# Kernel tuning notes

Hardware: AMD Instinct MI355X
Metric: run time of the kernel (lower is better)

## Reference

```python
import jax, jax.numpy as jnp
import numpy as np

H = 16
EPS = 1e-6
AUX_COEF = 0.01
TOPK = 2


def _rmsnorm(x, w):
    ms = jnp.mean(x * x, axis=-1, keepdims=True)
    return x * jax.lax.rsqrt(ms + EPS) * w


def _rope(t, cos, sin):
    # t: [B,H,T,hd]; cos/sin: [T, hd//2]
    half = t.shape[-1] // 2
    t1, t2 = t[..., :half], t[..., half:]
    return jnp.concatenate([t1 * cos - t2 * sin, t1 * sin + t2 * cos], axis=-1)


def setup_inputs() -> dict:
    key = jax.random.key(0)
    ks = jax.random.split(key, 16)
    B, T, D = 2, 1024, 1024
    E, I = 8, 4096
    s = lambda k, shp, fan: jax.random.normal(k, shp, dtype=jnp.float32) * (1.0 / np.sqrt(fan))
    return {
        "x": jax.random.normal(ks[0], (B, T, D), dtype=jnp.float32),
        "qkv_w": s(ks[1], (3 * D, D), D),
        "qkv_b": jnp.zeros((3 * D,), jnp.float32),
        "out_w": s(ks[2], (D, D), D),
        "out_b": jnp.zeros((D,), jnp.float32),
        "ln1_w": jnp.ones((D,), jnp.float32),
        "ln2_w": jnp.ones((D,), jnp.float32),
        "gate_w": s(ks[3], (E, D), D),
        "ew1": s(ks[4], (E, I, D), D),
        "eb1": jnp.zeros((E, I), jnp.float32),
        "ew2": s(ks[5], (E, D, I), I),
        "eb2": jnp.zeros((E, D), jnp.float32),
        "ew3": s(ks[6], (E, I, D), D),
        "eb3": jnp.zeros((E, I), jnp.float32),
    }


def _attention(x, qkv_w, qkv_b, out_w, out_b):
    B, T, D = x.shape
    hd = D // H
    half = hd // 2
    qkv = (x @ qkv_w.T + qkv_b).reshape(B, T, H, 3, hd)
    q = jnp.transpose(qkv[..., 0, :], (0, 2, 1, 3))  # [B,H,T,hd]
    k = jnp.transpose(qkv[..., 1, :], (0, 2, 1, 3))
    v = jnp.transpose(qkv[..., 2, :], (0, 2, 1, 3))
    theta = 1.0 / (10000.0 ** (jnp.arange(half, dtype=jnp.float32) / half))
    freq = jnp.arange(T, dtype=jnp.float32)[:, None] * theta[None, :]  # [T,half]
    cos, sin = jnp.cos(freq), jnp.sin(freq)
    q = _rope(q, cos, sin)
    k = _rope(k, cos, sin)
    # NOTE: original scales by embed_dim**-0.5 (not head_dim**-0.5)
    scale = D ** (-0.5)
    scores = jnp.einsum("bhqd,bhkd->bhqk", q, k) * scale
    mask = jnp.triu(jnp.full((T, T), -1e9, dtype=scores.dtype), k=1)
    w = jax.nn.softmax(scores + mask, axis=-1)
    attn = jnp.einsum("bhqk,bhkd->bhqd", w, v)
    attn = jnp.transpose(attn, (0, 2, 1, 3)).reshape(B, T, D)
    return attn @ out_w.T + out_b


def _moe(x, gate_w, ew1, eb1, ew2, eb2, ew3, eb3):
    B, T, D = x.shape
    E = gate_w.shape[0]
    xf = x.reshape(-1, D)  # [N,D]
    N = xf.shape[0]
    probs = jax.nn.softmax(xf @ gate_w.T, axis=-1)  # [N,E]
    topk_vals, topk_idx = jax.lax.top_k(probs, TOPK)
    oh = jax.nn.one_hot(topk_idx, E, dtype=xf.dtype)  # [N,K,E]
    gates = jnp.sum(oh * topk_vals[..., None], axis=1)  # [N,E] dense gate, zero off top-k
    # per-expert SwiGLU over all tokens, combined with sparse gates
    h = jax.nn.silu(jnp.einsum("nd,eid->nei", xf, ew1) + eb1) * (
        jnp.einsum("nd,eid->nei", xf, ew3) + eb3
    )  # [N,E,I]
    out_e = jnp.einsum("nei,edi->ned", h, ew2) + eb2  # [N,E,D]
    y = jnp.einsum("ned,ne->nd", out_e, gates)
    counts = jnp.sum(oh, axis=(0, 1))  # bincount of routed assignments
    f = counts / (N * TOPK)
    P = jnp.mean(probs, axis=0)
    aux = AUX_COEF * E * jnp.dot(f, P)
    return y.reshape(B, T, D), aux


def reference(x, qkv_w, qkv_b, out_w, out_b, ln1_w, ln2_w, gate_w, ew1, eb1, ew2, eb2, ew3, eb3):
    h1 = x + _attention(_rmsnorm(x, ln1_w), qkv_w, qkv_b, out_w, out_b)
    y, aux = _moe(_rmsnorm(h1, ln2_w), gate_w, ew1, eb1, ew2, eb2, ew3, eb3)
    return h1 + y, aux
```

## Files before the change

kernel.cpp:

```cpp
#include <hip/hip_runtime.h>
#include <cstdint>
#include <cstddef>
#include <math.h>

#define T_SEQ  1024
#define DMODEL 1024
#define NHEAD  16
#define HDIM   64
#define NEXP   8
#define IDIM   4096
#define NTOK   2048
#define NSLOT  4096

typedef short bf16x8 __attribute__((ext_vector_type(8)));
typedef short s16x4  __attribute__((ext_vector_type(4)));
typedef float floatx4 __attribute__((ext_vector_type(4)));
typedef unsigned int uintx4 __attribute__((ext_vector_type(4)));

__device__ __forceinline__ float bf2f(short s) {
  return __uint_as_float(((unsigned)(unsigned short)s) << 16);
}
__device__ __forceinline__ short f2bf(float f) {
  unsigned u = __float_as_uint(f);
  unsigned r = (u + 0x7FFFu + ((u >> 16) & 1u)) >> 16;
  return (short)r;
}
__device__ __forceinline__ unsigned cvt_pk_bf16(float lo, float hi) {
  unsigned r;
  asm("v_cvt_pk_bf16_f32 %0, %1, %2" : "=v"(r) : "v"(lo), "v"(hi));
  return r;
}
__device__ __forceinline__ uintx4 pack8_bf16(floatx4 a, floatx4 b) {
  uintx4 u;
  u[0] = cvt_pk_bf16(a[0], a[1]);
  u[1] = cvt_pk_bf16(a[2], a[3]);
  u[2] = cvt_pk_bf16(b[0], b[1]);
  u[3] = cvt_pk_bf16(b[2], b[3]);
  return u;
}
__device__ __forceinline__ void split8(const float* x, uintx4& hi, uintx4& lo) {
  #pragma unroll
  for (int i = 0; i < 4; i++) {
    unsigned h = cvt_pk_bf16(x[2*i], x[2*i+1]);
    hi[i] = h;
    float r0 = x[2*i]   - __uint_as_float(h << 16);
    float r1 = x[2*i+1] - __uint_as_float(h & 0xffff0000u);
    lo[i] = cvt_pk_bf16(r0, r1);
  }
}

__global__ __launch_bounds__(256) void rmsnorm_f32_kernel(
    const float* __restrict__ x, const float* __restrict__ w, float* __restrict__ out) {
  int row = blockIdx.x, tid = threadIdx.x;
  const floatx4* xr = (const floatx4*)(x + (size_t)row * DMODEL);
  floatx4 v = xr[tid];
  float ss = v[0]*v[0] + v[1]*v[1] + v[2]*v[2] + v[3]*v[3];
  #pragma unroll
  for (int off = 32; off > 0; off >>= 1) ss += __shfl_xor(ss, off);
  __shared__ float wsum[4];
  int wid = tid >> 6;
  if ((tid & 63) == 0) wsum[wid] = ss;
  __syncthreads();
  float tot = wsum[0] + wsum[1] + wsum[2] + wsum[3];
  float r = rsqrtf(tot * (1.0f / DMODEL) + 1e-6f);
  floatx4 wv = ((const floatx4*)w)[tid];
  floatx4 o;
  o[0] = v[0]*r*wv[0]; o[1] = v[1]*r*wv[1];
  o[2] = v[2]*r*wv[2]; o[3] = v[3]*r*wv[3];
  ((floatx4*)(out + (size_t)row * DMODEL))[tid] = o;
}

__global__ __launch_bounds__(256) void rmsnorm_bf16_kernel(
    const float* __restrict__ x, const float* __restrict__ w, short* __restrict__ out) {
  int row = blockIdx.x, tid = threadIdx.x;
  const floatx4* xr = (const floatx4*)(x + (size_t)row * DMODEL);
  floatx4 v = xr[tid];
  float ss = v[0]*v[0] + v[1]*v[1] + v[2]*v[2] + v[3]*v[3];
  #pragma unroll
  for (int off = 32; off > 0; off >>= 1) ss += __shfl_xor(ss, off);
  __shared__ float wsum[4];
  int wid = tid >> 6;
  if ((tid & 63) == 0) wsum[wid] = ss;
  __syncthreads();
  float tot = wsum[0] + wsum[1] + wsum[2] + wsum[3];
  float r = rsqrtf(tot * (1.0f / DMODEL) + 1e-6f);
  floatx4 wv = ((const floatx4*)w)[tid];
  s16x4 o;
  o[0] = f2bf(v[0]*r*wv[0]); o[1] = f2bf(v[1]*r*wv[1]);
  o[2] = f2bf(v[2]*r*wv[2]); o[3] = f2bf(v[3]*r*wv[3]);
  *(s16x4*)(out + (size_t)row * DMODEL + tid*4) = o;
}

template<int RESID>
__global__ __launch_bounds__(256) void gemm_3bf16(
    const float* __restrict__ A, const float* __restrict__ W,
    const float* __restrict__ bias, const float* __restrict__ resid,
    float* __restrict__ C, int N, int K) {
  __shared__ __attribute__((aligned(16))) short Ahi[64*40];
  __shared__ __attribute__((aligned(16))) short Alo[64*40];
  __shared__ __attribute__((aligned(16))) short Whi[64*40];
  __shared__ __attribute__((aligned(16))) short Wlo[64*40];
  int tid = threadIdx.x, lane = tid & 63, wid = tid >> 6;
  int wm = wid >> 1, wn = wid & 1;
  int m0 = blockIdx.y * 64, n0 = blockIdx.x * 64;
  floatx4 zero4 = {0.f,0.f,0.f,0.f};
  floatx4 acc[2][2];
  #pragma unroll
  for (int mi = 0; mi < 2; mi++)
    #pragma unroll
    for (int nj = 0; nj < 2; nj++) acc[mi][nj] = zero4;

  int ar = tid >> 2, ak = (tid & 3) * 8;
  const float* Ap = A + (size_t)(m0 + ar) * K + ak;
  const float* Wp = W + (size_t)(n0 + ar) * K + ak;
  int rsel = lane & 15, kseg = (lane >> 4) * 8;

  for (int kk = 0; kk < K; kk += 32) {
    float abuf[8], wbuf[8];
    *(floatx4*)(abuf)     = *(const floatx4*)(Ap + kk);
    *(floatx4*)(abuf + 4) = *(const floatx4*)(Ap + kk + 4);
    *(floatx4*)(wbuf)     = *(const floatx4*)(Wp + kk);
    *(floatx4*)(wbuf + 4) = *(const floatx4*)(Wp + kk + 4);
    uintx4 ahi, alo, whi, wlo;
    split8(abuf, ahi, alo);
    split8(wbuf, whi, wlo);
    __syncthreads();
    *(uintx4*)(&Ahi[ar*40 + ak]) = ahi;
    *(uintx4*)(&Alo[ar*40 + ak]) = alo;
    *(uintx4*)(&Whi[ar*40 + ak]) = whi;
    *(uintx4*)(&Wlo[ar*40 + ak]) = wlo;
    __syncthreads();
    bf16x8 afh[2], afl[2], wfh[2], wfl[2];
    #pragma unroll
    for (int mi = 0; mi < 2; mi++) {
      int row = (wm*32 + mi*16 + rsel)*40 + kseg;
      afh[mi] = *(const bf16x8*)(&Ahi[row]);
      afl[mi] = *(const bf16x8*)(&Alo[row]);
    }
    #pragma unroll
    for (int nj = 0; nj < 2; nj++) {
      int row = (wn*32 + nj*16 + rsel)*40 + kseg;
      wfh[nj] = *(const bf16x8*)(&Whi[row]);
      wfl[nj] = *(const bf16x8*)(&Wlo[row]);
    }
    #pragma unroll
    for (int mi = 0; mi < 2; mi++)
      #pragma unroll
      for (int nj = 0; nj < 2; nj++) {
        acc[mi][nj] = __builtin_amdgcn_mfma_f32_16x16x32_bf16(afl[mi], wfh[nj], acc[mi][nj], 0, 0, 0);
        acc[mi][nj] = __builtin_amdgcn_mfma_f32_16x16x32_bf16(afh[mi], wfl[nj], acc[mi][nj], 0, 0, 0);
        acc[mi][nj] = __builtin_amdgcn_mfma_f32_16x16x32_bf16(afh[mi], wfh[nj], acc[mi][nj], 0, 0, 0);
      }
  }
  int rj = (lane >> 4) * 4, cn = lane & 15;
  #pragma unroll
  for (int mi = 0; mi < 2; mi++) {
    #pragma unroll
    for (int nj = 0; nj < 2; nj++) {
      int n = n0 + wn*32 + nj*16 + cn;
      float bn = bias[n];
      #pragma unroll
      for (int j = 0; j < 4; j++) {
        int m = m0 + wm*32 + mi*16 + rj + j;
        float v = acc[mi][nj][j] + bn;
        if (RESID) v += resid[(size_t)m * N + n];
        C[(size_t)m * N + n] = v;
      }
    }
  }
}

__global__ void rope_table_kernel(float* __restrict__ cost, float* __restrict__ sint) {
  int t = blockIdx.x, d = threadIdx.x;
  double theta = pow(10000.0, -(double)d / 32.0);
  double f = (double)t * theta;
  cost[t*32 + d] = (float)cos(f);
  sint[t*32 + d] = (float)sin(f);
}

__global__ __launch_bounds__(256) void rope_kernel(
    const float* __restrict__ qkv, const float* __restrict__ cost, const float* __restrict__ sint,
    float* __restrict__ qr, float* __restrict__ kr) {
  int wid = threadIdx.x >> 6, lane = threadIdx.x & 63;
  int idx = blockIdx.x * 4 + wid;
  int h = idx & 15, n = idx >> 4;
  int t = n & (T_SEQ - 1), b = n >> 10;
  const float* base = qkv + (size_t)n * 3072 + h * 192;
  int d2 = lane & 31;
  float c = cost[t*32 + d2], s = sint[t*32 + d2];
  float q1 = base[d2],      q2 = base[d2 + 32];
  float k1 = base[64 + d2], k2 = base[96 + d2];
  float qo = (lane < 32) ? (q1*c - q2*s) : (q1*s + q2*c);
  float ko = (lane < 32) ? (k1*c - k2*s) : (k1*s + k2*c);
  size_t orow = ((size_t)(b*NHEAD + h) * T_SEQ + t) * HDIM;
  qr[orow + lane] = qo;
  kr[orow + lane] = ko;
}

__global__ __launch_bounds__(256) void vtrans_kernel(
    const float* __restrict__ qkvf, float* __restrict__ vrT) {
  __shared__ __attribute__((aligned(16))) float tile[64][68];
  int bh = blockIdx.x, t0 = blockIdx.y * 64;
  int b = bh >> 4, h = bh & 15;
  int tid = threadIdx.x;
  int r = tid >> 2, seg = (tid & 3) * 16;
  const float* src = qkvf + ((size_t)(b*T_SEQ + t0 + r))*3072 + h*192 + 128 + seg;
  floatx4 v0 = *(const floatx4*)(src);
  floatx4 v1 = *(const floatx4*)(src + 4);
  floatx4 v2 = *(const floatx4*)(src + 8);
  floatx4 v3 = *(const floatx4*)(src + 12);
  *(floatx4*)(&tile[r][seg])      = v0;
  *(floatx4*)(&tile[r][seg + 4])  = v1;
  *(floatx4*)(&tile[r][seg + 8])  = v2;
  *(floatx4*)(&tile[r][seg + 12]) = v3;
  __syncthreads();
  int dr = r, tseg = seg;
  floatx4 o0, o1, o2, o3;
  #pragma unroll
  for (int i = 0; i < 4; i++) {
    o0[i] = tile[tseg + i][dr];
    o1[i] = tile[tseg + 4 + i][dr];
    o2[i] = tile[tseg + 8 + i][dr];
    o3[i] = tile[tseg + 12 + i][dr];
  }
  float* dst = vrT + ((size_t)(bh*HDIM + dr))*T_SEQ + t0 + tseg;
  *(floatx4*)(dst)      = o0;
  *(floatx4*)(dst + 4)  = o1;
  *(floatx4*)(dst + 8)  = o2;
  *(floatx4*)(dst + 12) = o3;
}

__global__ __launch_bounds__(256) void attn_mfma_kernel(
    const float* __restrict__ qr_, const float* __restrict__ kr_,
    const float* __restrict__ vrT_, float* __restrict__ attno) {
  __shared__ __attribute__((aligned(16))) short Qhi[64*72];
  __shared__ __attribute__((aligned(16))) short Qlo[64*72];
  __shared__ __attribute__((aligned(16))) short Khi[64*72];
  __shared__ __attribute__((aligned(16))) short Klo[64*72];
  __shared__ __attribute__((aligned(16))) short Vhi[64*72];
  __shared__ __attribute__((aligned(16))) short Vlo[64*72];
  __shared__ __attribute__((aligned(16))) unsigned Pp[64*68];
  int tid = threadIdx.x, lane = tid & 63, w = tid >> 6;
  int bh = blockIdx.x;
  int qt = 15 - (int)blockIdx.y;
  int q0 = qt * 64;
  int b = bh >> 4, h = bh & 15;
  const float* Qb  = qr_  + ((size_t)bh * T_SEQ + q0) * HDIM;
  const float* Kb  = kr_  + (size_t)bh * T_SEQ * HDIM;
  const float* Vtb = vrT_ + (size_t)bh * HDIM * T_SEQ;

  int srow = tid >> 2, sseg = (tid & 3) * 16;
  {
    const float* src = Qb + srow*HDIM + sseg;
    float b0[8], b1[8];
    *(floatx4*)(b0)   = *(const floatx4*)(src);
    *(floatx4*)(b0+4) = *(const floatx4*)(src + 4);
    *(floatx4*)(b1)   = *(const floatx4*)(src + 8);
    *(floatx4*)(b1+4) = *(const floatx4*)(src + 12);
    uintx4 h0, l0, h1, l1;
    split8(b0, h0, l0); split8(b1, h1, l1);
    *(uintx4*)(&Qhi[srow*72 + sseg])     = h0;
    *(uintx4*)(&Qhi[srow*72 + sseg + 8]) = h1;
    *(uintx4*)(&Qlo[srow*72 + sseg])     = l0;
    *(uintx4*)(&Qlo[srow*72 + sseg + 8]) = l1;
  }

  int rsel = lane & 15, kseg = (lane >> 4) * 8, cl = lane & 15;
  int rbase = w*16 + (lane >> 4) * 4;
  const float scale = 0.03125f;
  float mrow[4] = {-1e30f,-1e30f,-1e30f,-1e30f};
  float lrow[4] = {0.f,0.f,0.f,0.f};
  floatx4 zero4 = {0.f,0.f,0.f,0.f};
  floatx4 Of[4];
  #pragma unroll
  for (int f = 0; f < 4; f++) Of[f] = zero4;

  int ntiles = qt + 1;
  for (int kt = 0; kt < ntiles; kt++) {
    int kbase = kt << 6;
    const float* kp = Kb  + (size_t)(kbase + srow)*HDIM + sseg;
    const float* vp = Vtb + (size_t)srow*T_SEQ + kbase + sseg;
    float kb0[8], kb1[8], vb0[8], vb1[8];
    *(floatx4*)(kb0)   = *(const floatx4*)(kp);
    *(floatx4*)(kb0+4) = *(const floatx4*)(kp + 4);
    *(floatx4*)(kb1)   = *(const floatx4*)(kp + 8);
    *(floatx4*)(kb1+4) = *(const floatx4*)(kp + 12);
    *(floatx4*)(vb0)   = *(const floatx4*)(vp);
    *(floatx4*)(vb0+4) = *(const floatx4*)(vp + 4);
    *(floatx4*)(vb1)   = *(const floatx4*)(vp + 8);
    *(floatx4*)(vb1+4) = *(const floatx4*)(vp + 12);
    __syncthreads();
    {
      uintx4 h0, l0, h1, l1;
      split8(kb0, h0, l0); split8(kb1, h1, l1);
      *(uintx4*)(&Khi[srow*72 + sseg])     = h0;
      *(uintx4*)(&Khi[srow*72 + sseg + 8]) = h1;
      *(uintx4*)(&Klo[srow*72 + sseg])     = l0;
      *(uintx4*)(&Klo[srow*72 + sseg + 8]) = l1;
      split8(vb0, h0, l0); split8(vb1, h1, l1);
      *(uintx4*)(&Vhi[srow*72 + sseg])     = h0;
      *(uintx4*)(&Vhi[srow*72 + sseg + 8]) = h1;
      *(uintx4*)(&Vlo[srow*72 + sseg])     = l0;
      *(uintx4*)(&Vlo[srow*72 + sseg + 8]) = l1;
    }
    __syncthreads();
    floatx4 sf[4];
    #pragma unroll
    for (int f = 0; f < 4; f++) sf[f] = zero4;
    #pragma unroll
    for (int c = 0; c < 2; c++) {
      int ko = c*32 + kseg;
      bf16x8 qh = *(const bf16x8*)(&Qhi[(w*16 + rsel)*72 + ko]);
      bf16x8 ql = *(const bf16x8*)(&Qlo[(w*16 + rsel)*72 + ko]);
      #pragma unroll
      for (int f = 0; f < 4; f++) {
        bf16x8 kh = *(const bf16x8*)(&Khi[(f*16 + rsel)*72 + ko]);
        bf16x8 kl = *(const bf16x8*)(&Klo[(f*16 + rsel)*72 + ko]);
        sf[f] = __builtin_amdgcn_mfma_f32_16x16x32_bf16(ql, kh, sf[f], 0, 0, 0);
        sf[f] = __builtin_amdgcn_mfma_f32_16x16x32_bf16(qh, kl, sf[f], 0, 0, 0);
        sf[f] = __builtin_amdgcn_mfma_f32_16x16x32_bf16(qh, kh, sf[f], 0, 0, 0);
      }
    }
    float pm[4] = {-1e30f,-1e30f,-1e30f,-1e30f};
    #pragma unroll
    for (int f = 0; f < 4; f++) {
      int col = kbase + f*16 + cl;
      #pragma unroll
      for (int j = 0; j < 4; j++) {
        float s = sf[f][j];
        s = (col <= q0 + rbase + j) ? s*scale : -1e30f;
        sf[f][j] = s;
        pm[j] = fmaxf(pm[j], s);
      }
    }
    #pragma unroll
    for (int off = 1; off < 16; off <<= 1)
      #pragma unroll
      for (int j = 0; j < 4; j++) pm[j] = fmaxf(pm[j], __shfl_xor(pm[j], off));
    float sc[4], rs[4] = {0.f,0.f,0.f,0.f};
    #pragma unroll
    for (int j = 0; j < 4; j++) {
      float mn = fmaxf(mrow[j], pm[j]);
      sc[j] = __expf(mrow[j] - mn);
      mrow[j] = mn;
    }
    #pragma unroll
    for (int f = 0; f < 4; f++) {
      #pragma unroll
      for (int j = 0; j < 4; j++) {
        float p = (sf[f][j] > -1e29f) ? __expf(sf[f][j] - mrow[j]) : 0.f;
        rs[j] += p;
        unsigned hp = cvt_pk_bf16(p, 0.f);
        float ph = __uint_as_float(hp << 16);
        unsigned lp = cvt_pk_bf16(p - ph, 0.f);
        Pp[(rbase + j)*68 + f*16 + cl] = (hp << 16) | (lp & 0xffffu);
      }
    }
    #pragma unroll
    for (int off = 1; off < 16; off <<= 1)
      #pragma unroll
      for (int j = 0; j < 4; j++) rs[j] += __shfl_xor(rs[j], off);
    #pragma unroll
    for (int j = 0; j < 4; j++) lrow[j] = lrow[j]*sc[j] + rs[j];
    #pragma unroll
    for (int f = 0; f < 4; f++)
      #pragma unroll
      for (int j = 0; j < 4; j++) Of[f][j] *= sc[j];
    __syncthreads();
    #pragma unroll
    for (int c = 0; c < 2; c++) {
      int prow = (w*16 + rsel)*68 + c*32 + kseg;
      uintx4 d0 = *(const uintx4*)(&Pp[prow]);
      uintx4 d1 = *(const uintx4*)(&Pp[prow + 4]);
      uintx4 phw, plw;
      phw[0] = (d0[0] >> 16) | (d0[1] & 0xffff0000u);
      phw[1] = (d0[2] >> 16) | (d0[3] & 0xffff0000u);
      phw[2] = (d1[0] >> 16) | (d1[1] & 0xffff0000u);
      phw[3] = (d1[2] >> 16) | (d1[3] & 0xffff0000u);
      plw[0] = (d0[0] & 0xffffu) | (d0[1] << 16);
      plw[1] = (d0[2] & 0xffffu) | (d0[3] << 16);
      plw[2] = (d1[0] & 0xffffu) | (d1[1] << 16);
      plw[3] = (d1[2] & 0xffffu) | (d1[3] << 16);
      bf16x8 Ph = *(bf16x8*)&phw;
      bf16x8 Pl = *(bf16x8*)&plw;
      int ko = c*32 + kseg;
      #pragma unroll
      for (int f = 0; f < 4; f++) {
        bf16x8 vh = *(const bf16x8*)(&Vhi[(f*16 + rsel)*72 + ko]);
        bf16x8 vl = *(const bf16x8*)(&Vlo[(f*16 + rsel)*72 + ko]);
        Of[f] = __builtin_amdgcn_mfma_f32_16x16x32_bf16(Pl, vh, Of[f], 0, 0, 0);
        Of[f] = __builtin_amdgcn_mfma_f32_16x16x32_bf16(Ph, vl, Of[f], 0, 0, 0);
        Of[f] = __builtin_amdgcn_mfma_f32_16x16x32_bf16(Ph, vh, Of[f], 0, 0, 0);
      }
    }
  }
  #pragma unroll
  for (int j = 0; j < 4; j++) {
    float inv = 1.0f / lrow[j];
    size_t rowoff = ((size_t)(b*T_SEQ + q0 + rbase + j))*DMODEL + h*HDIM;
    #pragma unroll
    for (int f = 0; f < 4; f++)
      attno[rowoff + f*16 + cl] = Of[f][j] * inv;
  }
}

__global__ __launch_bounds__(64) void gate_kernel(
    const float* __restrict__ h1, const float* __restrict__ lnw, const float* __restrict__ gw,
    float* __restrict__ probs, int* __restrict__ pair, float* __restrict__ gpair,
    int* __restrict__ counts) {
  int n = blockIdx.x, lane = threadIdx.x;
  const float* xp = h1 + (size_t)n * DMODEL + lane*16;
  float xv[16];
  double ss = 0.0;
  #pragma unroll
  for (int j = 0; j < 16; j++) { xv[j] = xp[j]; ss += (double)xv[j] * (double)xv[j]; }
  #pragma unroll
  for (int off = 32; off > 0; off >>= 1) ss += __shfl_xor(ss, off);
  double r = 1.0 / sqrt(ss * (1.0 / DMODEL) + 1e-6);
  const float* wp = lnw + lane*16;
  double xf[16];
  #pragma unroll
  for (int j = 0; j < 16; j++) xf[j] = (double)xv[j] * r * (double)wp[j];
  double logit[8];
  #pragma unroll
  for (int e = 0; e < 8; e++) {
    const float* g = gw + e*DMODEL + lane*16;
    double acc = 0.0;
    #pragma unroll
    for (int j = 0; j < 16; j++) acc += xf[j] * (double)g[j];
    logit[e] = acc;
  }
  #pragma unroll
  for (int e = 0; e < 8; e++)
    #pragma unroll
    for (int off = 32; off > 0; off >>= 1) logit[e] += __shfl_xor(logit[e], off);
  double mxl = logit[0];
  #pragma unroll
  for (int e = 1; e < 8; e++) mxl = fmax(mxl, logit[e]);
  double p[8], Z = 0.0;
  #pragma unroll
  for (int e = 0; e < 8; e++) { p[e] = exp(logit[e] - mxl); Z += p[e]; }
  double invZ = 1.0 / Z;
  #pragma unroll
  for (int e = 0; e < 8; e++) p[e] *= invZ;
  int e0 = 0; double b0 = p[0];
  #pragma unroll
  for (int e = 1; e < 8; e++) if (p[e] > b0) { b0 = p[e]; e0 = e; }
  int e1 = -1; double b1 = -1.0;
  #pragma unroll
  for (int e = 0; e < 8; e++) if (e != e0 && p[e] > b1) { b1 = p[e]; e1 = e; }
  if (lane == 0) {
    #pragma unroll
    for (int e = 0; e < 8; e++) probs[n*8 + e] = (float)p[e];
    pair[2*n] = e0; pair[2*n+1] = e1;
    gpair[2*n] = (float)b0; gpair[2*n+1] = (float)b1;
    atomicAdd(&counts[e0], 1);
    atomicAdd(&counts[e1], 1);
  }
}

__global__ void offsets_kernel(const int* __restrict__ counts, int* __restrict__ off,
                               int* __restrict__ cursor) {
  if (threadIdx.x == 0) {
    int a = 0;
    for (int e = 0; e < 8; e++) { off[e] = a; cursor[e] = a; a += counts[e]; }
    off[8] = a;
  }
}

__global__ __launch_bounds__(256) void scatter_kernel(
    const int* __restrict__ pair, const float* __restrict__ gpair, int* __restrict__ cursor,
    int* __restrict__ tok_of_slot, float* __restrict__ gate_of_slot, int* __restrict__ slot_of_tok) {
  int n = blockIdx.x * 256 + threadIdx.x;
  int e0 = pair[2*n], e1 = pair[2*n+1];
  int s0 = atomicAdd(&cursor[e0], 1);
  tok_of_slot[s0] = n; gate_of_slot[s0] = gpair[2*n];   slot_of_tok[2*n] = s0;
  int s1 = atomicAdd(&cursor[e1], 1);
  tok_of_slot[s1] = n; gate_of_slot[s1] = gpair[2*n+1]; slot_of_tok[2*n+1] = s1;
}

__global__ __launch_bounds__(256) void aux_kernel(
    const float* __restrict__ probs, const int* __restrict__ counts, float* __restrict__ outaux) {
  __shared__ double sm[256];
  int t = threadIdx.x;
  int e = t & 7, base = t >> 3;
  double acc = 0.0;
  for (int n = base; n < NTOK; n += 32) acc += (double)probs[n*8 + e];
  sm[t] = acc;
  __syncthreads();
  if (t < 8) {
    double s = 0.0;
    for (int g = 0; g < 32; g++) s += sm[g*8 + t];
    sm[t] = s;
  }
  __syncthreads();
  if (t == 0) {
    double aux = 0.0;
    for (int ee = 0; ee < 8; ee++)
      aux += ((double)counts[ee] * (1.0 / (NTOK*2))) * (sm[ee] * (1.0 / NTOK));
    outaux[0] = (float)(0.08 * aux);
  }
}

__global__ __launch_bounds__(256) void moe13_kernel(
    const short* __restrict__ xn2,
    const float* __restrict__ ew1, const float* __restrict__ eb1,
    const float* __restrict__ ew3, const float* __restrict__ eb3,
    const int* __restrict__ counts, const int* __restrict__ off,
    const int* __restrict__ tok_of_slot, short* __restrict__ hbuf) {
  int e = blockIdx.z;
  int Me = counts[e];
  int m0 = blockIdx.y * 128;
  if (m0 >= Me) return;
  int base = off[e];
  int i0 = blockIdx.x * 64;
  __shared__ __attribute__((aligned(16))) short As[2][128*40];
  __shared__ __attribute__((aligned(16))) short W1s[2][64*40];
  __shared__ __attribute__((aligned(16))) short W3s[2][64*40];
  int tid = threadIdx.x, lane = tid & 63, wid = tid >> 6;
  int wm = wid >> 1, wn = wid & 1;
  floatx4 zero4 = {0.f,0.f,0.f,0.f};
  floatx4 acc1[4][2], acc3[4][2];
  #pragma unroll
  for (int mi = 0; mi < 4; mi++)
    #pragma unroll
    for (int nj = 0; nj < 2; nj++) { acc1[mi][nj] = zero4; acc3[mi][nj] = zero4; }

  int ar = tid >> 1, ak = (tid & 1) * 8;
  int am = m0 + ar;
  bool aval = (am < Me);
  const short* Ag = xn2 + (size_t)(aval ? tok_of_slot[base + am] : 0) * DMODEL;
  int wr = tid >> 2, wk = (tid & 3) * 8;
  const float* W1g = ew1 + ((size_t)e*IDIM + i0 + wr)*DMODEL + wk;
  const float* W3g = ew3 + ((size_t)e*IDIM + i0 + wr)*DMODEL + wk;
  int rsel = lane & 15, kseg = (lane >> 4) * 8;

  {
    bf16x8 a0 = {0,0,0,0,0,0,0,0}, a1 = {0,0,0,0,0,0,0,0};
    if (aval) {
      a0 = *(const bf16x8*)(Ag + ak);
      a1 = *(const bf16x8*)(Ag + ak + 16);
    }
    floatx4 u0 = *(const floatx4*)(W1g);
    floatx4 u1 = *(const floatx4*)(W1g + 4);
    floatx4 v0 = *(const floatx4*)(W3g);
    floatx4 v1 = *(const floatx4*)(W3g + 4);
    *(bf16x8*)(&As[0][ar*40 + ak])      = a0;
    *(bf16x8*)(&As[0][ar*40 + ak + 16]) = a1;
    *(uintx4*)(&W1s[0][wr*40 + wk]) = pack8_bf16(u0, u1);
    *(uintx4*)(&W3s[0][wr*40 + wk]) = pack8_bf16(v0, v1);
  }
  __syncthreads();

  for (int kk = 0; kk < DMODEL; kk += 32) {
    int cur = (kk >> 5) & 1;
    int nxt = cur ^ 1;
    bool more = (kk + 32 < DMODEL);
    bf16x8 na0 = {0,0,0,0,0,0,0,0}, na1 = {0,0,0,0,0,0,0,0};
    floatx4 nu0, nu1, nv0, nv1;
    if (more) {
      if (aval) {
        na0 = *(const bf16x8*)(Ag + kk + 32 + ak);
        na1 = *(const bf16x8*)(Ag + kk + 32 + ak + 16);
      }
      nu0 = *(const floatx4*)(W1g + kk + 32);
      nu1 = *(const floatx4*)(W1g + kk + 36);
      nv0 = *(const floatx4*)(W3g + kk + 32);
      nv1 = *(const floatx4*)(W3g + kk + 36);
    }
    bf16x8 af[4], w1f[2], w3f[2];
    #pragma unroll
    for (int mi = 0; mi < 4; mi++)
      af[mi] = *(const bf16x8*)(&As[cur][(wm*64 + mi*16 + rsel)*40 + kseg]);
    #pragma unroll
    for (int nj = 0; nj < 2; nj++) {
      w1f[nj] = *(const bf16x8*)(&W1s[cur][(wn*32 + nj*16 + rsel)*40 + kseg]);
      w3f[nj] = *(const bf16x8*)(&W3s[cur][(wn*32 + nj*16 + rsel)*40 + kseg]);
    }
    #pragma unroll
    for (int mi = 0; mi < 4; mi++)
      #pragma unroll
      for (int nj = 0; nj < 2; nj++) {
        acc1[mi][nj] = __builtin_amdgcn_mfma_f32_16x16x32_bf16(af[mi], w1f[nj], acc1[mi][nj], 0, 0, 0);
        acc3[mi][nj] = __builtin_amdgcn_mfma_f32_16x16x32_bf16(af[mi], w3f[nj], acc3[mi][nj], 0, 0, 0);
      }
    if (more) {
      *(bf16x8*)(&As[nxt][ar*40 + ak])      = na0;
      *(bf16x8*)(&As[nxt][ar*40 + ak + 16]) = na1;
      *(uintx4*)(&W1s[nxt][wr*40 + wk]) = pack8_bf16(nu0, nu1);
      *(uintx4*)(&W3s[nxt][wr*40 + wk]) = pack8_bf16(nv0, nv1);
    }
    __syncthreads();
  }
  int rj = (lane >> 4) * 4, cn = lane & 15;
  #pragma unroll
  for (int mi = 0; mi < 4; mi++) {
    #pragma unroll
    for (int nj = 0; nj < 2; nj++) {
      int i = i0 + wn*32 + nj*16 + cn;
      float be1 = eb1[e*IDIM + i], be3 = eb3[e*IDIM + i];
      #pragma unroll
      for (int j = 0; j < 4; j++) {
        int m = m0 + wm*64 + mi*16 + rj + j;
        if (m < Me) {
          float a = acc1[mi][nj][j] + be1;
          float b = acc3[mi][nj][j] + be3;
          float hval = (a / (1.f + __expf(-a))) * b;
          hbuf[(size_t)(base + m)*IDIM + i] = f2bf(hval);
        }
      }
    }
  }
}

__global__ __launch_bounds__(256) void moe2_kernel(
    const short* __restrict__ hbuf, const float* __restrict__ ew2, const float* __restrict__ eb2,
    const int* __restrict__ counts, const int* __restrict__ off,
    const float* __restrict__ gate_of_slot,
    float* __restrict__ y0, float* __restrict__ y1) {
  int e = blockIdx.z;
  int Me = counts[e];
  int m0 = blockIdx.y * 128;
  if (m0 >= Me) return;
  int base = off[e];
  int n0 = (blockIdx.x & 7) * 128;
  int khalf = blockIdx.x >> 3;
  int kbeg = khalf * (IDIM/2);
  __shared__ __attribute__((aligned(16))) short As[2][128*40];
  __shared__ __attribute__((aligned(16))) short Ws[2][128*40];
  int tid = threadIdx.x, lane = tid & 63, wid = tid >> 6;
  int wm = wid >> 1, wn = wid & 1;
  floatx4 zero4 = {0.f,0.f,0.f,0.f};
  floatx4 acc[4][4];
  #pragma unroll
  for (int mi = 0; mi < 4; mi++)
    #pragma unroll
    for (int nj = 0; nj < 4; nj++) acc[mi][nj] = zero4;

  int ar = tid >> 1, ak = (tid & 1) * 8, kw = (tid & 1) * 16;
  bool aval = (m0 + ar) < Me;
  const short* Ag = hbuf + (size_t)(base + (aval ? (m0 + ar) : 0)) * IDIM + kbeg;
  const float* Wg = ew2 + ((size_t)e*DMODEL + n0 + ar)*IDIM + kbeg;
  int rsel = lane & 15, kseg = (lane >> 4) * 8;

  {
    bf16x8 a0 = {0,0,0,0,0,0,0,0}, a1 = {0,0,0,0,0,0,0,0};
    if (aval) {
      a0 = *(const bf16x8*)(Ag + ak);
      a1 = *(const bf16x8*)(Ag + ak + 16);
    }
    floatx4 w0 = *(const floatx4*)(Wg + kw);
    floatx4 w1 = *(const floatx4*)(Wg + kw + 4);
    floatx4 w2 = *(const floatx4*)(Wg + kw + 8);
    floatx4 w3 = *(const floatx4*)(Wg + kw + 12);
    *(bf16x8*)(&As[0][ar*40 + ak])      = a0;
    *(bf16x8*)(&As[0][ar*40 + ak + 16]) = a1;
    *(uintx4*)(&Ws[0][ar*40 + kw])     = pack8_bf16(w0, w1);
    *(uintx4*)(&Ws[0][ar*40 + kw + 8]) = pack8_bf16(w2, w3);
  }
  __syncthreads();

  for (int kk = 0; kk < IDIM/2; kk += 32) {
    int cur = (kk >> 5) & 1;
    int nxt = cur ^ 1;
    bool more = (kk + 32 < IDIM/2);
    bf16x8 na0 = {0,0,0,0,0,0,0,0}, na1 = {0,0,0,0,0,0,0,0};
    floatx4 nw0, nw1, nw2, nw3;
    if (more) {
      if (aval) {
        na0 = *(const bf16x8*)(Ag + kk + 32 + ak);
        na1 = *(const bf16x8*)(Ag + kk + 32 + ak + 16);
      }
      nw0 = *(const floatx4*)(Wg + kk + 32 + kw);
      nw1 = *(const floatx4*)(Wg + kk + 32 + kw + 4);
      nw2 = *(const floatx4*)(Wg + kk + 32 + kw + 8);
      nw3 = *(const floatx4*)(Wg + kk + 32 + kw + 12);
    }
    bf16x8 af[4], wf[4];
    #pragma unroll
    for (int mi = 0; mi < 4; mi++)
      af[mi] = *(const bf16x8*)(&As[cur][(wm*64 + mi*16 + rsel)*40 + kseg]);
    #pragma unroll
    for (int nj = 0; nj < 4; nj++)
      wf[nj] = *(const bf16x8*)(&Ws[cur][(wn*64 + nj*16 + rsel)*40 + kseg]);
    #pragma unroll
    for (int mi = 0; mi < 4; mi++)
      #pragma unroll
      for (int nj = 0; nj < 4; nj++)
        acc[mi][nj] = __builtin_amdgcn_mfma_f32_16x16x32_bf16(af[mi], wf[nj], acc[mi][nj], 0, 0, 0);
    if (more) {
      *(bf16x8*)(&As[nxt][ar*40 + ak])      = na0;
      *(bf16x8*)(&As[nxt][ar*40 + ak + 16]) = na1;
      *(uintx4*)(&Ws[nxt][ar*40 + kw])     = pack8_bf16(nw0, nw1);
      *(uintx4*)(&Ws[nxt][ar*40 + kw + 8]) = pack8_bf16(nw2, nw3);
    }
    __syncthreads();
  }
  int rj = (lane >> 4) * 4, cn = lane & 15;
  float* yout = khalf ? y1 : y0;
  #pragma unroll
  for (int mi = 0; mi < 4; mi++) {
    #pragma unroll
    for (int nj = 0; nj < 4; nj++) {
      int n = n0 + wn*64 + nj*16 + cn;
      float bn = khalf ? 0.f : eb2[e*DMODEL + n];
      #pragma unroll
      for (int j = 0; j < 4; j++) {
        int m = m0 + wm*64 + mi*16 + rj + j;
        if (m < Me) {
          float g = gate_of_slot[base + m];
          yout[(size_t)(base + m)*DMODEL + n] = (acc[mi][nj][j] + bn) * g;
        }
      }
    }
  }
}

__global__ __launch_bounds__(256) void combine_kernel(
    const float* __restrict__ h1, const float* __restrict__ y0, const float* __restrict__ y1,
    const int* __restrict__ slot_of_tok, float* __restrict__ out) {
  int n = blockIdx.x, t = threadIdx.x;
  int sA = slot_of_tok[2*n], sB = slot_of_tok[2*n+1];
  const floatx4* a   = (const floatx4*)(h1 + (size_t)n*DMODEL);
  const floatx4* y0a = (const floatx4*)(y0 + (size_t)sA*DMODEL);
  const floatx4* y1a = (const floatx4*)(y1 + (size_t)sA*DMODEL);
  const floatx4* y0b = (const floatx4*)(y0 + (size_t)sB*DMODEL);
  const floatx4* y1b = (const floatx4*)(y1 + (size_t)sB*DMODEL);
  floatx4 v = a[t] + (y0a[t] + y1a[t]) + (y0b[t] + y1b[t]);
  ((floatx4*)(out + (size_t)n*DMODEL))[t] = v;
}

extern "C" void kernel_launch(void* const* d_in, const int* in_sizes, int n_in,
                              void* d_out, int out_size, void* d_ws, size_t ws_size,
                              hipStream_t stream) {
  const float* x      = (const float*)d_in[0];
  const float* qkv_w  = (const float*)d_in[1];
  const float* qkv_b  = (const float*)d_in[2];
  const float* out_w  = (const float*)d_in[3];
  const float* out_b  = (const float*)d_in[4];
  const float* ln1_w  = (const float*)d_in[5];
  const float* ln2_w  = (const float*)d_in[6];
  const float* gate_w = (const float*)d_in[7];
  const float* ew1    = (const float*)d_in[8];
  const float* eb1    = (const float*)d_in[9];
  const float* ew2    = (const float*)d_in[10];
  const float* eb2    = (const float*)d_in[11];
  const float* ew3    = (const float*)d_in[12];
  const float* eb3    = (const float*)d_in[13];
  float* out = (float*)d_out;

  char* ws = (char*)d_ws;
  float* xn1f   = (float*)(ws + 0);
  float* attnof = (float*)(ws + 0);
  float* qkvf   = (float*)(ws + 8388608);
  float* h1     = (float*)(ws + 8388608);
  short* xn2    = (short*)(ws + 16777216);
  float* yslot1 = (float*)(ws + 16777216);
  float* qrf    = (float*)(ws + 33554432);
  float* krf    = (float*)(ws + 41943040);
  float* vrT    = (float*)(ws + 50331648);
  short* hbuf   = (short*)(ws + 33554432);
  float* yslot0 = (float*)(ws + 67108864);
  float* cost         = (float*)(ws + 83886080);
  float* sint         = (float*)(ws + 84017152);
  float* probs        = (float*)(ws + 84148224);
  int*   ctrl         = (int*)  (ws + 84213760);
  int*   pair         = (int*)  (ws + 84214784);
  float* gpair        = (float*)(ws + 84231168);
  int*   slot_of_tok  = (int*)  (ws + 84247552);
  int*   tok_of_slot  = (int*)  (ws + 84263936);
  float* gate_of_slot = (float*)(ws + 84280320);

  int* counts = ctrl;
  int* off    = ctrl + 8;
  int* cursor = ctrl + 20;

  hipMemsetAsync(ctrl, 0, 1024, stream);
  rope_table_kernel<<<T_SEQ, 32, 0, stream>>>(cost, sint);
  rmsnorm_f32_kernel<<<NTOK, 256, 0, stream>>>(x, ln1_w, xn1f);
  gemm_3bf16<0><<<dim3(48, 32), 256, 0, stream>>>(xn1f, qkv_w, qkv_b, nullptr, qkvf, 3072, DMODEL);
  rope_kernel<<<8192, 256, 0, stream>>>(qkvf, cost, sint, qrf, krf);
  vtrans_kernel<<<dim3(32, 16), 256, 0, stream>>>(qkvf, vrT);
  attn_mfma_kernel<<<dim3(32, 16), 256, 0, stream>>>(qrf, krf, vrT, attnof);
  gemm_3bf16<1><<<dim3(16, 32), 256, 0, stream>>>(attnof, out_w, out_b, x, h1, DMODEL, DMODEL);
  rmsnorm_bf16_kernel<<<NTOK, 256, 0, stream>>>(h1, ln2_w, xn2);
  gate_kernel<<<NTOK, 64, 0, stream>>>(h1, ln2_w, gate_w, probs, pair, gpair, counts);
  offsets_kernel<<<1, 64, 0, stream>>>(counts, off, cursor);
  scatter_kernel<<<8, 256, 0, stream>>>(pair, gpair, cursor, tok_of_slot, gate_of_slot, slot_of_tok);
  aux_kernel<<<1, 256, 0, stream>>>(probs, counts, out + 2097152);
  moe13_kernel<<<dim3(64, 16, 8), 256, 0, stream>>>(xn2, ew1, eb1, ew3, eb3, counts, off, tok_of_slot, hbuf);
  moe2_kernel<<<dim3(16, 16, 8), 256, 0, stream>>>(hbuf, ew2, eb2, counts, off, gate_of_slot, yslot0, yslot1);
  combine_kernel<<<NTOK, 256, 0, stream>>>(h1, yslot0, yslot1, slot_of_tok, out);
}
```

Baseline: 540.1 us.

## Double-buffer LDS tiles in split-bf16 GEMM to overlap global loads with MFMA

Adds ping-pong shared-memory buffers to the 3xbf16 GEMM. The next K-slice is prefetched into registers before the MFMAs on the current slice, then split and stored into the other buffer, so each iteration needs one barrier instead of two. The aim is to hide global load latency behind compute, at the cost of double the LDS footprint, which may lower occupancy.

```diff
diff --git a/kernel.cpp b/kernel.cpp
--- a/kernel.cpp
+++ b/kernel.cpp
@@ -96,10 +96,10 @@
     const float* __restrict__ A, const float* __restrict__ W,
     const float* __restrict__ bias, const float* __restrict__ resid,
     float* __restrict__ C, int N, int K) {
-  __shared__ __attribute__((aligned(16))) short Ahi[64*40];
-  __shared__ __attribute__((aligned(16))) short Alo[64*40];
-  __shared__ __attribute__((aligned(16))) short Whi[64*40];
-  __shared__ __attribute__((aligned(16))) short Wlo[64*40];
+  __shared__ __attribute__((aligned(16))) short Ahi[2][64*40];
+  __shared__ __attribute__((aligned(16))) short Alo[2][64*40];
+  __shared__ __attribute__((aligned(16))) short Whi[2][64*40];
+  __shared__ __attribute__((aligned(16))) short Wlo[2][64*40];
   int tid = threadIdx.x, lane = tid & 63, wid = tid >> 6;
   int wm = wid >> 1, wn = wid & 1;
   int m0 = blockIdx.y * 64, n0 = blockIdx.x * 64;
@@ -115,33 +115,45 @@
   const float* Wp = W + (size_t)(n0 + ar) * K + ak;
   int rsel = lane & 15, kseg = (lane >> 4) * 8;
 
-  for (int kk = 0; kk < K; kk += 32) {
+  {
     float abuf[8], wbuf[8];
-    *(floatx4*)(abuf)     = *(const floatx4*)(Ap + kk);
-    *(floatx4*)(abuf + 4) = *(const floatx4*)(Ap + kk + 4);
-    *(floatx4*)(wbuf)     = *(const floatx4*)(Wp + kk);
-    *(floatx4*)(wbuf + 4) = *(const floatx4*)(Wp + kk + 4);
+    *(floatx4*)(abuf)     = *(const floatx4*)(Ap);
+    *(floatx4*)(abuf + 4) = *(const floatx4*)(Ap + 4);
+    *(floatx4*)(wbuf)     = *(const floatx4*)(Wp);
+    *(floatx4*)(wbuf + 4) = *(const floatx4*)(Wp + 4);
     uintx4 ahi, alo, whi, wlo;
     split8(abuf, ahi, alo);
     split8(wbuf, whi, wlo);
-    __syncthreads();
-    *(uintx4*)(&Ahi[ar*40 + ak]) = ahi;
-    *(uintx4*)(&Alo[ar*40 + ak]) = alo;
-    *(uintx4*)(&Whi[ar*40 + ak]) = whi;
-    *(uintx4*)(&Wlo[ar*40 + ak]) = wlo;
-    __syncthreads();
+    *(uintx4*)(&Ahi[0][ar*40 + ak]) = ahi;
+    *(uintx4*)(&Alo[0][ar*40 + ak]) = alo;
+    *(uintx4*)(&Whi[0][ar*40 + ak]) = whi;
+    *(uintx4*)(&Wlo[0][ar*40 + ak]) = wlo;
+  }
+  __syncthreads();
+
+  for (int kk = 0; kk < K; kk += 32) {
+    int cur = (kk >> 5) & 1;
+    int nxt = cur ^ 1;
+    bool more = (kk + 32 < K);
+    float nab[8], nwb[8];
+    if (more) {
+      *(floatx4*)(nab)     = *(const floatx4*)(Ap + kk + 32);
+      *(floatx4*)(nab + 4) = *(const floatx4*)(Ap + kk + 36);
+      *(floatx4*)(nwb)     = *(const floatx4*)(Wp + kk + 32);
+      *(floatx4*)(nwb + 4) = *(const floatx4*)(Wp + kk + 36);
+    }
     bf16x8 afh[2], afl[2], wfh[2], wfl[2];
     #pragma unroll
     for (int mi = 0; mi < 2; mi++) {
       int row = (wm*32 + mi*16 + rsel)*40 + kseg;
-      afh[mi] = *(const bf16x8*)(&Ahi[row]);
-      afl[mi] = *(const bf16x8*)(&Alo[row]);
+      afh[mi] = *(const bf16x8*)(&Ahi[cur][row]);
+      afl[mi] = *(const bf16x8*)(&Alo[cur][row]);
     }
     #pragma unroll
     for (int nj = 0; nj < 2; nj++) {
       int row = (wn*32 + nj*16 + rsel)*40 + kseg;
-      wfh[nj] = *(const bf16x8*)(&Whi[row]);
-      wfl[nj] = *(const bf16x8*)(&Wlo[row]);
+      wfh[nj] = *(const bf16x8*)(&Whi[cur][row]);
+      wfl[nj] = *(const bf16x8*)(&Wlo[cur][row]);
     }
     #pragma unroll
     for (int mi = 0; mi < 2; mi++)
@@ -151,6 +163,16 @@
         acc[mi][nj] = __builtin_amdgcn_mfma_f32_16x16x32_bf16(afh[mi], wfl[nj], acc[mi][nj], 0, 0, 0);
         acc[mi][nj] = __builtin_amdgcn_mfma_f32_16x16x32_bf16(afh[mi], wfh[nj], acc[mi][nj], 0, 0, 0);
       }
+    if (more) {
+      uintx4 ahi, alo, whi, wlo;
+      split8(nab, ahi, alo);
+      split8(nwb, whi, wlo);
+      *(uintx4*)(&Ahi[nxt][ar*40 + ak]) = ahi;
+      *(uintx4*)(&Alo[nxt][ar*40 + ak]) = alo;
+      *(uintx4*)(&Whi[nxt][ar*40 + ak]) = whi;
+      *(uintx4*)(&Wlo[nxt][ar*40 + ak]) = wlo;
+    }
+    __syncthreads();
   }
   int rj = (lane >> 4) * 4, cn = lane & 15;
   #pragma unroll
```

Measured after the change: 536.1 us, median of 4. No clear change (-0.7%).
